# Performance work log

Hardware: AMD Instinct MI355X
Metric: run time of the kernel (lower is better)

## Reference

```python
import jax, jax.numpy as jnp
import numpy as np
from jax import lax

B, N, F_, K, C = 16, 64, 1024, 13, 2   # batch, channels, feat(time), conv kernel, classes
EPS_BN = 1e-5


def setup_inputs() -> dict:
    key = jax.random.key(0)
    ks = jax.random.split(key, 12)
    kf = 1.0 / np.sqrt(F_)   # torch uniform init bound for Linear(F,.) and w
    kn = 1.0 / np.sqrt(N)    # Conv1d(N,1,k=1) bound
    kk = 1.0 / np.sqrt(K)    # Conv1d(1,1,k=K) bound
    u = lambda k, shape, b: jax.random.uniform(k, shape, jnp.float32, -b, b)
    return {
        "x": jax.random.normal(ks[0], (B, N, F_), jnp.float32),
        "w": u(ks[1], (F_,), kf),
        "gin_W": u(ks[2], (F_, F_), kf),
        "gin_b": u(ks[3], (F_,), kf),
        "bn1_g": jnp.ones((N,), jnp.float32),
        "bn1_b": jnp.zeros((N,), jnp.float32),
        "lc_W": u(ks[4], (N,), kn),
        "lc_b": u(ks[5], (1,), kn),
        "conv_W": u(ks[6], (1, 1, K), kk),
        "conv_b": u(ks[7], (1,), kk),
        "bn2_g": jnp.ones((1,), jnp.float32),
        "bn2_b": jnp.zeros((1,), jnp.float32),
        "out_W": u(ks[8], (C, F_), kf),
        "out_b": u(ks[9], (C,), kf),
    }


def reference(x, w, gin_W, gin_b, bn1_g, bn1_b, lc_W, lc_b, conv_W, conv_b,
              bn2_g, bn2_b, out_W, out_b):
    # --- learned adjacency: weighted L1 pairwise score ---
    diff = jnp.abs(x[:, :, None, :] - x[:, None, :, :])        # [B,N,N,F] big intermediate
    s = jnp.einsum('bijf,f->bij', diff, w)                      # [B,N,N]
    s = -jax.nn.relu(s)
    adj = jax.nn.softmax(s, axis=1)                             # softmax over dim 1 (as torch)
    # --- GIN aggregation (eps=0): (adj + I) @ x, then Linear ---
    a = adj + jnp.eye(N, dtype=x.dtype)
    h = jnp.einsum('bij,bjf->bif', a, x)                        # [B,N,F]
    h = jnp.einsum('bif,of->bio', h, gin_W) + gin_b             # [B,N,F]
    # --- BatchNorm1d over channels (train-mode batch stats, biased var) ---
    m = h.mean(axis=(0, 2), keepdims=True)
    v = h.var(axis=(0, 2), keepdims=True)
    h = (h - m) / jnp.sqrt(v + EPS_BN) * bn1_g[None, :, None] + bn1_b[None, :, None]
    # --- Conv1d(N->1, k=1): channel mixing ---
    y = jnp.einsum('bnf,n->bf', h, lc_W) + lc_b                 # [B,F]
    # --- Conv1d(1->1, k=K, padding='same') ---
    y = lax.conv_general_dilated(y[:, None, :], conv_W, (1,), 'SAME') + conv_b[None, :, None]
    # --- BatchNorm1d(1) ---
    m2 = y.mean(axis=(0, 2), keepdims=True)
    v2 = y.var(axis=(0, 2), keepdims=True)
    y = (y - m2) / jnp.sqrt(v2 + EPS_BN) * bn2_g[None, :, None] + bn2_b[None, :, None]
    # --- head ---
    y = jax.nn.relu(y.reshape(B, F_))
    logits = y @ out_W.T + out_b                                # [B,C]
    return jax.nn.softmax(logits, axis=1), adj
```

## Files before the change

### kernel.cpp

```cpp
#include <hip/hip_runtime.h>
#include <hip/hip_bf16.h>


typedef __attribute__((ext_vector_type(8))) __bf16 bf16x8;
typedef __attribute__((ext_vector_type(4))) float f32x4;

__device__ __forceinline__ unsigned short f2bf(float f) {
  union { float f; unsigned int u; } v; v.f = f;
  unsigned int r = v.u + 0x7FFFu + ((v.u >> 16) & 1u);
  return (unsigned short)(r >> 16);
}

__global__ __launch_bounds__(256) void k1_spart_gemm(
    const float* __restrict__ x, const float* __restrict__ w,
    const float* __restrict__ gin_W,
    float* __restrict__ spart, float* __restrict__ gpart,
    unsigned* __restrict__ bar) {
  __shared__ __align__(16) union {
    struct { float xt[64 * 68]; float wt[64]; } s;
    struct { unsigned short A[64 * 72]; unsigned short B[64 * 72]; } g;
  } sm;
  int t = threadIdx.x, bid = blockIdx.x;

  if (bid == 0 && t == 0) *bar = 0u;

  if (bid >= 512) {
    int sbid = bid - 512;
    int b = sbid >> 4, ft = sbid & 15, f0 = ft * 64;
    const float4* pf = reinterpret_cast<const float4*>(gin_W) + (size_t)sbid * 1024 + t;
    float4 pf0 = pf[0], pf1 = pf[256], pf2 = pf[512], pf3 = pf[768];
    for (int c = 0; c < 16; ++c) {
      int idx = c * 256 + t;
      int n = idx >> 6, f = idx & 63;
      sm.s.xt[n * 68 + f] = x[b * 65536 + n * 1024 + f0 + f];
    }
    if (t < 64) sm.s.wt[t] = w[f0 + t];
    __syncthreads();
    asm volatile("" :: "v"(pf0.x), "v"(pf1.x), "v"(pf2.x), "v"(pf3.x));
    int i0 = (t >> 4) * 4, j0 = (t & 15) * 4;
    float acc[4][4];
#pragma unroll
    for (int ii = 0; ii < 4; ++ii)
#pragma unroll
      for (int jj = 0; jj < 4; ++jj) acc[ii][jj] = 0.f;
    for (int f = 0; f < 64; f += 4) {
      float4 wv = *reinterpret_cast<const float4*>(&sm.s.wt[f]);
      float4 av[4], bv[4];
#pragma unroll
      for (int ii = 0; ii < 4; ++ii) av[ii] = *reinterpret_cast<const float4*>(&sm.s.xt[(i0 + ii) * 68 + f]);
#pragma unroll
      for (int jj = 0; jj < 4; ++jj) bv[jj] = *reinterpret_cast<const float4*>(&sm.s.xt[(j0 + jj) * 68 + f]);
#pragma unroll
      for (int ii = 0; ii < 4; ++ii)
#pragma unroll
        for (int jj = 0; jj < 4; ++jj) {
          acc[ii][jj] += fabsf(av[ii].x - bv[jj].x) * wv.x
                       + fabsf(av[ii].y - bv[jj].y) * wv.y
                       + fabsf(av[ii].z - bv[jj].z) * wv.z
                       + fabsf(av[ii].w - bv[jj].w) * wv.w;
        }
    }
    float* out = spart + (size_t)sbid * 4096;
#pragma unroll
    for (int ii = 0; ii < 4; ++ii)
#pragma unroll
      for (int jj = 0; jj < 4; ++jj)
        out[(ii + i0) * 64 + (j0 + jj)] = acc[ii][jj];
    return;
  }

  int g = bid;
  int xcd = g & 7, idx = g >> 3;
  int lt = idx & 31, slice = idx >> 5;
  int tr = 4 * (xcd & 3) + (lt >> 3);
  int tc = 8 * (xcd >> 2) + (lt & 7);
  int k0 = slice * 512;
  int wave = t >> 6, lane = t & 63;
  int wr = wave * 16;
  int lrow = lane & 15, kg = lane >> 4;
  f32x4 acc[4];
#pragma unroll
  for (int nj = 0; nj < 4; ++nj) acc[nj] = f32x4{0.f, 0.f, 0.f, 0.f};

  for (int chunk = 0; chunk < 8; ++chunk) {
    int kc = k0 + chunk * 64;
#pragma unroll
    for (int u = 0; u < 4; ++u) {
      int idx4 = u * 256 + t;
      int row = idx4 >> 4, kq = idx4 & 15;
      float4 va = *reinterpret_cast<const float4*>(&x[(size_t)(tr * 64 + row) * 1024 + kc + kq * 4]);
      ushort4 ua; ua.x = f2bf(va.x); ua.y = f2bf(va.y); ua.z = f2bf(va.z); ua.w = f2bf(va.w);
      *reinterpret_cast<ushort4*>(&sm.g.A[row * 72 + kq * 4]) = ua;
    }
#pragma unroll
    for (int u = 0; u < 4; ++u) {
      int idx4 = u * 256 + t;
      int row = idx4 >> 4, kq = idx4 & 15;
      float4 vb = *reinterpret_cast<const float4*>(&gin_W[(size_t)(tc * 64 + row) * 1024 + kc + kq * 4]);
      ushort4 ub; ub.x = f2bf(vb.x); ub.y = f2bf(vb.y); ub.z = f2bf(vb.z); ub.w = f2bf(vb.w);
      *reinterpret_cast<ushort4*>(&sm.g.B[row * 72 + kq * 4]) = ub;
    }
    __syncthreads();
#pragma unroll
    for (int ks = 0; ks < 2; ++ks) {
      bf16x8 a = *reinterpret_cast<const bf16x8*>(&sm.g.A[(wr + lrow) * 72 + ks * 32 + kg * 8]);
      bf16x8 bf_[4];
#pragma unroll
      for (int nj = 0; nj < 4; ++nj)
        bf_[nj] = *reinterpret_cast<const bf16x8*>(&sm.g.B[(nj * 16 + lrow) * 72 + ks * 32 + kg * 8]);
#pragma unroll
      for (int nj = 0; nj < 4; ++nj)
        acc[nj] = __builtin_amdgcn_mfma_f32_16x16x32_bf16(a, bf_[nj], acc[nj], 0, 0, 0);
    }
    __syncthreads();
  }
  float* gp = gpart + (size_t)slice * (1024u * 1024u);
#pragma unroll
  for (int nj = 0; nj < 4; ++nj) {
    int row = tr * 64 + wr + kg * 4;
    int col = tc * 64 + nj * 16 + lrow;
#pragma unroll
    for (int r = 0; r < 4; ++r)
      gp[(size_t)(row + r) * 1024 + col] = acc[nj][r];
  }
}

__global__ __launch_bounds__(512) void k2_adj_h2(
    const float* __restrict__ spart, const float* __restrict__ gpart,
    const float* __restrict__ gin_b,
    float* __restrict__ dout, float* __restrict__ h2, float* __restrict__ part) {
  __shared__ float adjs[64 * 65];
  __shared__ float csum[32][64];
  __shared__ float cinv[64];
  __shared__ __align__(16) float gt[64 * 68];
  int t = threadIdx.x, bid = blockIdx.x;
  int xcd = bid & 7, local = bid >> 3;
  int b = (xcd << 1) | (local & 1);
  int ft = local >> 1;
  int f0 = ft * 64;
  {
    int i = t >> 4, fl = (t & 15) * 4;
#pragma unroll
    for (int c = 0; c < 2; ++c) {
      int row = c * 32 + i;
      const float* base = gpart + (size_t)(b * 64 + row) * 1024 + f0 + fl;
      float4 s0 = *reinterpret_cast<const float4*>(base);
      float4 s1 = *reinterpret_cast<const float4*>(base + (1u << 20));
      float4 g4;
      g4.x = s0.x + s1.x; g4.y = s0.y + s1.y;
      g4.z = s0.z + s1.z; g4.w = s0.w + s1.w;
      *reinterpret_cast<float4*>(&gt[row * 68 + fl]) = g4;
    }
  }
  int tj = t & 15, tr2 = t >> 4;
  float4 v4[2];
#pragma unroll
  for (int r = 0; r < 2; ++r) v4[r] = make_float4(0.f, 0.f, 0.f, 0.f);
  for (int ft2 = 0; ft2 < 16; ++ft2) {
    const float* p = spart + (size_t)(b * 16 + ft2) * 4096 + tj * 4;
#pragma unroll
    for (int r = 0; r < 2; ++r) {
      float4 s = *reinterpret_cast<const float4*>(&p[(tr2 * 2 + r) * 64]);
      v4[r].x += s.x; v4[r].y += s.y; v4[r].z += s.z; v4[r].w += s.w;
    }
  }
  float4 colsum = make_float4(0.f, 0.f, 0.f, 0.f);
#pragma unroll
  for (int r = 0; r < 2; ++r) {
    float4 e;
    e.x = expf(-fmaxf(v4[r].x, 0.f));
    e.y = expf(-fmaxf(v4[r].y, 0.f));
    e.z = expf(-fmaxf(v4[r].z, 0.f));
    e.w = expf(-fmaxf(v4[r].w, 0.f));
    int row = tr2 * 2 + r;
    adjs[row * 65 + tj * 4 + 0] = e.x;
    adjs[row * 65 + tj * 4 + 1] = e.y;
    adjs[row * 65 + tj * 4 + 2] = e.z;
    adjs[row * 65 + tj * 4 + 3] = e.w;
    colsum.x += e.x; colsum.y += e.y; colsum.z += e.z; colsum.w += e.w;
  }
  csum[tr2][tj * 4 + 0] = colsum.x;
  csum[tr2][tj * 4 + 1] = colsum.y;
  csum[tr2][tj * 4 + 2] = colsum.z;
  csum[tr2][tj * 4 + 3] = colsum.w;
  __syncthreads();
  if (t < 64) {
    float s = 0.f;
#pragma unroll
    for (int g2 = 0; g2 < 32; ++g2) s += csum[g2][t];
    cinv[t] = 1.f / s;
  }
  __syncthreads();
  float* doutAdj = dout + 32 + (size_t)b * 4096;
#pragma unroll
  for (int r = 0; r < 2; ++r) {
    int row = tr2 * 2 + r;
#pragma unroll
    for (int c = 0; c < 4; ++c) {
      int col = tj * 4 + c;
      float a = adjs[row * 65 + col] * cinv[col];
      adjs[row * 65 + col] = a;
      if (ft == 0) doutAdj[row * 64 + col] = a;
    }
  }
  __syncthreads();
  int i0 = (t >> 4) * 2, fl = (t & 15) * 4;
  float4 gbv = *reinterpret_cast<const float4*>(&gin_b[f0 + fl]);
  float4 acc4[2];
  acc4[0] = *reinterpret_cast<const float4*>(&gt[i0 * 68 + fl]);
  acc4[1] = *reinterpret_cast<const float4*>(&gt[(i0 + 1) * 68 + fl]);
  for (int j = 0; j < 64; ++j) {
    float4 gv = *reinterpret_cast<const float4*>(&gt[j * 68 + fl]);
    float a0 = adjs[i0 * 65 + j], a1 = adjs[(i0 + 1) * 65 + j];
    acc4[0].x += a0 * gv.x; acc4[0].y += a0 * gv.y; acc4[0].z += a0 * gv.z; acc4[0].w += a0 * gv.w;
    acc4[1].x += a1 * gv.x; acc4[1].y += a1 * gv.y; acc4[1].z += a1 * gv.z; acc4[1].w += a1 * gv.w;
  }
  float rs[2], rq[2];
#pragma unroll
  for (int ii = 0; ii < 2; ++ii) {
    acc4[ii].x += gbv.x; acc4[ii].y += gbv.y; acc4[ii].z += gbv.z; acc4[ii].w += gbv.w;
    *reinterpret_cast<float4*>(&h2[(size_t)(b * 64 + i0 + ii) * 1024 + f0 + fl]) = acc4[ii];
    rs[ii] = (acc4[ii].x + acc4[ii].y) + (acc4[ii].z + acc4[ii].w);
    rq[ii] = (acc4[ii].x * acc4[ii].x + acc4[ii].y * acc4[ii].y)
           + (acc4[ii].z * acc4[ii].z + acc4[ii].w * acc4[ii].w);
  }
#pragma unroll
  for (int m = 1; m < 16; m <<= 1) {
#pragma unroll
    for (int r = 0; r < 2; ++r) {
      rs[r] += __shfl_xor(rs[r], m, 64);
      rq[r] += __shfl_xor(rq[r], m, 64);
    }
  }
  if ((t & 15) == 0) {
    float* pp = part + (size_t)(b * 16 + ft) * 128;
#pragma unroll
    for (int r = 0; r < 2; ++r) {
      int n = i0 + r;
      pp[2 * n]     = rs[r];
      pp[2 * n + 1] = rq[r];
    }
  }
}

__global__ __launch_bounds__(256) void k3_y_head(
    const float* __restrict__ h2, const float* __restrict__ part,
    const float* __restrict__ lc_W, const float* __restrict__ lc_b,
    const float* __restrict__ bn1_g, const float* __restrict__ bn1_b,
    const float* __restrict__ conv_W, const float* __restrict__ conv_b,
    const float* __restrict__ bn2_g, const float* __restrict__ bn2_b,
    const float* __restrict__ out_W, const float* __restrict__ out_b,
    float* __restrict__ y2, float* __restrict__ bn2part,
    float* __restrict__ dout, unsigned* __restrict__ bar) {
  __shared__ float redp[2][128];
  __shared__ float cls[64], dds[64];
  __shared__ float yloc[268];
  __shared__ float red[256], red2[256];
  __shared__ float c0s;
  __shared__ unsigned tk;
  int t = threadIdx.x, bid = blockIdx.x;
  int b = ((bid & 7) << 1) | ((bid >> 3) & 1);
  int fq = bid >> 4;
  int f0 = fq * 256;
  {
    int k = t & 127, h = t >> 7;
    float s = 0.f;
    const float* pp = part + (size_t)h * 128 * 128 + k;
    for (int p = 0; p < 128; ++p) s += pp[(size_t)p * 128];
    redp[h][k] = s;
  }
  __syncthreads();
  if (t < 64) {
    float sum = redp[0][2 * t] + redp[1][2 * t];
    float sq  = redp[0][2 * t + 1] + redp[1][2 * t + 1];
    float m = sum * (1.f / 16384.f);
    float var = sq * (1.f / 16384.f) - m * m;
    float inv = 1.f / sqrtf(var + 1e-5f);
    float g = bn1_g[t], be = bn1_b[t], lw = lc_W[t];
    cls[t] = lw * g * inv;
    dds[t] = lw * (be - m * inv * g);
  }
  __syncthreads();
  if (t == 0) {
    float s = 0.f;
    for (int n = 0; n < 64; ++n) s += dds[n];
    c0s = s + lc_b[0];
  }
  __syncthreads();
  float c0 = c0s;
  for (int idx = t; idx < 268; idx += 256) {
    int f = f0 - 6 + idx;
    float acc = 0.f;
    if (f >= 0 && f < 1024) {
      acc = c0;
      const float* col = h2 + (size_t)(b * 64) * 1024 + f;
      for (int n = 0; n < 64; ++n) acc += cls[n] * col[(size_t)n * 1024];
    }
    yloc[idx] = acc;
  }
  __syncthreads();
  float cw[13];
#pragma unroll
  for (int k = 0; k < 13; ++k) cw[k] = conv_W[k];
  float vv = conv_b[0];
#pragma unroll
  for (int k = 0; k < 13; ++k) vv += yloc[t + k] * cw[k];
  y2[b * 1024 + f0 + t] = vv;
  red[t] = vv; red2[t] = vv * vv;
  __syncthreads();
  for (int off = 128; off > 0; off >>= 1) {
    if (t < off) { red[t] += red[t + off]; red2[t] += red2[t + off]; }
    __syncthreads();
  }
  if (t == 0) {
    int dchunk = b * 4 + fq;
    bn2part[2 * dchunk] = red[0]; bn2part[2 * dchunk + 1] = red2[0];
  }

  __syncthreads();
  if (t == 0) { __threadfence(); tk = atomicAdd(bar, 1u); }
  __syncthreads();
  if (tk != 63u) return;
  __threadfence();

  {
    float S = 0.f, S2 = 0.f;
    for (int i = 0; i < 64; ++i) { S += bn2part[2 * i]; S2 += bn2part[2 * i + 1]; }
    float m2 = S * (1.f / 16384.f);
    float inv2 = 1.f / sqrtf(S2 * (1.f / 16384.f) - m2 * m2 + 1e-5f);
    float g2 = bn2_g[0] * inv2, be2 = bn2_b[0];
    int hb = t >> 4, seg = t & 15;
    const float4* yv = reinterpret_cast<const float4*>(&y2[hb * 1024 + seg * 64]);
    const float4* w0 = reinterpret_cast<const float4*>(&out_W[seg * 64]);
    const float4* w1 = reinterpret_cast<const float4*>(&out_W[1024 + seg * 64]);
    float a0 = 0.f, a1 = 0.f;
#pragma unroll 4
    for (int u = 0; u < 16; ++u) {
      float4 y4 = yv[u], cc0 = w0[u], cc1 = w1[u];
      float vx = fmaxf((y4.x - m2) * g2 + be2, 0.f);
      float vy = fmaxf((y4.y - m2) * g2 + be2, 0.f);
      float vz = fmaxf((y4.z - m2) * g2 + be2, 0.f);
      float vw = fmaxf((y4.w - m2) * g2 + be2, 0.f);
      a0 += vx * cc0.x + vy * cc0.y + vz * cc0.z + vw * cc0.w;
      a1 += vx * cc1.x + vy * cc1.y + vz * cc1.z + vw * cc1.w;
    }
    red[t] = a0; red2[t] = a1;
    __syncthreads();
    for (int off = 8; off > 0; off >>= 1) {
      if (seg < off) { red[t] += red[t + off]; red2[t] += red2[t + off]; }
      __syncthreads();
    }
    if (seg == 0) {
      float l0 = red[t] + out_b[0], l1 = red2[t] + out_b[1];
      float mx = fmaxf(l0, l1);
      float e0 = expf(l0 - mx), e1 = expf(l1 - mx);
      float inv = 1.f / (e0 + e1);
      dout[hb * 2 + 0] = e0 * inv;
      dout[hb * 2 + 1] = e1 * inv;
    }
  }
}

extern "C" void kernel_launch(void* const* d_in, const int* in_sizes, int n_in,
                              void* d_out, int out_size, void* d_ws, size_t ws_size,
                              hipStream_t stream) {
  (void)in_sizes; (void)n_in; (void)out_size; (void)ws_size;
  const float* x      = (const float*)d_in[0];
  const float* w      = (const float*)d_in[1];
  const float* gin_W  = (const float*)d_in[2];
  const float* gin_b  = (const float*)d_in[3];
  const float* bn1_g  = (const float*)d_in[4];
  const float* bn1_b  = (const float*)d_in[5];
  const float* lc_W   = (const float*)d_in[6];
  const float* lc_b   = (const float*)d_in[7];
  const float* conv_W = (const float*)d_in[8];
  const float* conv_b = (const float*)d_in[9];
  const float* bn2_g  = (const float*)d_in[10];
  const float* bn2_b  = (const float*)d_in[11];
  const float* out_W  = (const float*)d_in[12];
  const float* out_b  = (const float*)d_in[13];
  float* dout = (float*)d_out;

  char* ws = (char*)d_ws;
  float* spart   = (float*)ws;
  float* h2      = (float*)(ws + (4u << 20));
  float* gpart   = (float*)(ws + (8u << 20));
  float* part    = (float*)(ws + (16u << 20));
  float* y2      = (float*)(ws + (16u << 20) + (128u << 10));
  float* bn2part = (float*)(ws + (16u << 20) + (192u << 10));
  unsigned* bar  = (unsigned*)(ws + (16u << 20) + (194u << 10));

  k1_spart_gemm<<<dim3(768), dim3(256), 0, stream>>>(x, w, gin_W, spart, gpart, bar);
  k2_adj_h2    <<<dim3(256), dim3(512), 0, stream>>>(spart, gpart, gin_b, dout, h2, part);
  k3_y_head    <<<dim3(64),  dim3(256), 0, stream>>>(h2, part, lc_W, lc_b, bn1_g, bn1_b,
                                                     conv_W, conv_b, bn2_g, bn2_b, out_W, out_b,
                                                     y2, bn2part, dout, bar);
}
```

Measured before the change: 64.01 us.

## Move BN1 stat reduction into k2 last-block and widen k3 grid

```diff
diff --git a/kernel.cpp b/kernel.cpp
--- a/kernel.cpp
+++ b/kernel.cpp
@@ -22,7 +22,7 @@
   } sm;
   int t = threadIdx.x, bid = blockIdx.x;
 
-  if (bid == 0 && t == 0) *bar = 0u;
+  if (bid == 0 && t == 0) { bar[0] = 0u; bar[16] = 0u; }
 
   if (bid >= 512) {
     int sbid = bid - 512;
@@ -65,7 +65,7 @@
     for (int ii = 0; ii < 4; ++ii)
 #pragma unroll
       for (int jj = 0; jj < 4; ++jj)
-        out[(ii + i0) * 64 + (j0 + jj)] = acc[ii][jj];
+        out[(i0 + ii) * 64 + (j0 + jj)] = acc[ii][jj];
     return;
   }
 
@@ -128,11 +128,14 @@
 __global__ __launch_bounds__(512) void k2_adj_h2(
     const float* __restrict__ spart, const float* __restrict__ gpart,
     const float* __restrict__ gin_b,
-    float* __restrict__ dout, float* __restrict__ h2, float* __restrict__ part) {
+    float* __restrict__ dout, float* __restrict__ h2, float* __restrict__ part,
+    float* __restrict__ stats, unsigned* __restrict__ bar) {
   __shared__ float adjs[64 * 65];
   __shared__ float csum[32][64];
   __shared__ float cinv[64];
   __shared__ __align__(16) float gt[64 * 68];
+  __shared__ float redps[4][128];
+  __shared__ unsigned tk;
   int t = threadIdx.x, bid = blockIdx.x;
   int xcd = bid & 7, local = bid >> 3;
   int b = (xcd << 1) | (local & 1);
@@ -241,10 +244,32 @@
       pp[2 * n + 1] = rq[r];
     }
   }
+
+  __syncthreads();
+  if (t == 0) { __threadfence(); tk = atomicAdd(&bar[16], 1u); }
+  __syncthreads();
+  if (tk != 255u) return;
+  __threadfence();
+  {
+    int slot = t & 127, quarter = t >> 7;
+    float s = 0.f;
+    const float* pp = part + (size_t)quarter * 64 * 128 + slot;
+    for (int p = 0; p < 64; ++p) s += pp[(size_t)p * 128];
+    redps[quarter][slot] = s;
+    __syncthreads();
+    if (t < 64) {
+      float sum = (redps[0][2 * t] + redps[1][2 * t]) + (redps[2][2 * t] + redps[3][2 * t]);
+      float sq  = (redps[0][2 * t + 1] + redps[1][2 * t + 1]) + (redps[2][2 * t + 1] + redps[3][2 * t + 1]);
+      float m = sum * (1.f / 16384.f);
+      float var = sq * (1.f / 16384.f) - m * m;
+      stats[2 * t]     = m;
+      stats[2 * t + 1] = 1.f / sqrtf(var + 1e-5f);
+    }
+  }
 }
 
 __global__ __launch_bounds__(256) void k3_y_head(
-    const float* __restrict__ h2, const float* __restrict__ part,
+    const float* __restrict__ h2, const float* __restrict__ stats,
     const float* __restrict__ lc_W, const float* __restrict__ lc_b,
     const float* __restrict__ bn1_g, const float* __restrict__ bn1_b,
     const float* __restrict__ conv_W, const float* __restrict__ conv_b,
@@ -252,30 +277,17 @@
     const float* __restrict__ out_W, const float* __restrict__ out_b,
     float* __restrict__ y2, float* __restrict__ bn2part,
     float* __restrict__ dout, unsigned* __restrict__ bar) {
-  __shared__ float redp[2][128];
   __shared__ float cls[64], dds[64];
-  __shared__ float yloc[268];
+  __shared__ float plds[4][76];
+  __shared__ float yloc[76];
   __shared__ float red[256], red2[256];
   __shared__ float c0s;
   __shared__ unsigned tk;
   int t = threadIdx.x, bid = blockIdx.x;
-  int b = ((bid & 7) << 1) | ((bid >> 3) & 1);
-  int fq = bid >> 4;
-  int f0 = fq * 256;
-  {
-    int k = t & 127, h = t >> 7;
-    float s = 0.f;
-    const float* pp = part + (size_t)h * 128 * 128 + k;
-    for (int p = 0; p < 128; ++p) s += pp[(size_t)p * 128];
-    redp[h][k] = s;
-  }
-  __syncthreads();
+  int b = bid >> 4, fq = bid & 15;
+  int f0 = fq * 64;
   if (t < 64) {
-    float sum = redp[0][2 * t] + redp[1][2 * t];
-    float sq  = redp[0][2 * t + 1] + redp[1][2 * t + 1];
-    float m = sum * (1.f / 16384.f);
-    float var = sq * (1.f / 16384.f) - m * m;
-    float inv = 1.f / sqrtf(var + 1e-5f);
+    float m = stats[2 * t], inv = stats[2 * t + 1];
     float g = bn1_g[t], be = bn1_b[t], lw = lc_W[t];
     cls[t] = lw * g * inv;
     dds[t] = lw * (be - m * inv * g);
@@ -287,48 +299,63 @@
     c0s = s + lc_b[0];
   }
   __syncthreads();
-  float c0 = c0s;
-  for (int idx = t; idx < 268; idx += 256) {
-    int f = f0 - 6 + idx;
-    float acc = 0.f;
-    if (f >= 0 && f < 1024) {
-      acc = c0;
-      const float* col = h2 + (size_t)(b * 64) * 1024 + f;
-      for (int n = 0; n < 64; ++n) acc += cls[n] * col[(size_t)n * 1024];
-    }
-    yloc[idx] = acc;
-  }
-  __syncthreads();
-  float cw[13];
-#pragma unroll
-  for (int k = 0; k < 13; ++k) cw[k] = conv_W[k];
-  float vv = conv_b[0];
-#pragma unroll
-  for (int k = 0; k < 13; ++k) vv += yloc[t + k] * cw[k];
-  y2[b * 1024 + f0 + t] = vv;
-  red[t] = vv; red2[t] = vv * vv;
-  __syncthreads();
-  for (int off = 128; off > 0; off >>= 1) {
-    if (t < off) { red[t] += red[t + off]; red2[t] += red2[t + off]; }
-    __syncthreads();
-  }
-  if (t == 0) {
-    int dchunk = b * 4 + fq;
-    bn2part[2 * dchunk] = red[0]; bn2part[2 * dchunk + 1] = red2[0];
-  }
-
-  __syncthreads();
-  if (t == 0) { __threadfence(); tk = atomicAdd(bar, 1u); }
-  __syncthreads();
-  if (tk != 63u) return;
+  {
+    int q = t >> 6, il = t & 63;
+    for (int idx = il; idx < 76; idx += 64) {
+      int f = f0 - 6 + idx;
+      float acc = 0.f;
+      if (f >= 0 && f < 1024) {
+        const float* col = h2 + (size_t)(b * 64) * 1024 + f;
+#pragma unroll
+        for (int n = 0; n < 16; ++n) acc += cls[q * 16 + n] * col[(size_t)(q * 16 + n) * 1024];
+      }
+      plds[q][idx] = acc;
+    }
+  }
+  __syncthreads();
+  if (t < 76) {
+    int f = f0 - 6 + t;
+    float v = 0.f;
+    if (f >= 0 && f < 1024)
+      v = c0s + ((plds[0][t] + plds[1][t]) + (plds[2][t] + plds[3][t]));
+    yloc[t] = v;
+  }
+  __syncthreads();
+  if (t < 64) {
+    float cw[13];
+#pragma unroll
+    for (int k = 0; k < 13; ++k) cw[k] = conv_W[k];
+    float vv = conv_b[0];
+#pragma unroll
+    for (int k = 0; k < 13; ++k) vv += yloc[t + k] * cw[k];
+    y2[b * 1024 + f0 + t] = vv;
+    float s = vv, s2 = vv * vv;
+#pragma unroll
+    for (int m = 1; m < 64; m <<= 1) {
+      s  += __shfl_xor(s, m, 64);
+      s2 += __shfl_xor(s2, m, 64);
+    }
+    if (t == 0) { bn2part[2 * bid] = s; bn2part[2 * bid + 1] = s2; }
+  }
+
+  __syncthreads();
+  if (t == 0) { __threadfence(); tk = atomicAdd(&bar[0], 1u); }
+  __syncthreads();
+  if (tk != 255u) return;
   __threadfence();
 
   {
-    float S = 0.f, S2 = 0.f;
-    for (int i = 0; i < 64; ++i) { S += bn2part[2 * i]; S2 += bn2part[2 * i + 1]; }
+    red[t] = bn2part[2 * t]; red2[t] = bn2part[2 * t + 1];
+    __syncthreads();
+    for (int off = 128; off > 0; off >>= 1) {
+      if (t < off) { red[t] += red[t + off]; red2[t] += red2[t + off]; }
+      __syncthreads();
+    }
+    float S = red[0], S2 = red2[0];
     float m2 = S * (1.f / 16384.f);
     float inv2 = 1.f / sqrtf(S2 * (1.f / 16384.f) - m2 * m2 + 1e-5f);
     float g2 = bn2_g[0] * inv2, be2 = bn2_b[0];
+    __syncthreads();
     int hb = t >> 4, seg = t & 15;
     const float4* yv = reinterpret_cast<const float4*>(&y2[hb * 1024 + seg * 64]);
     const float4* w0 = reinterpret_cast<const float4*>(&out_W[seg * 64]);
@@ -388,11 +415,13 @@
   float* part    = (float*)(ws + (16u << 20));
   float* y2      = (float*)(ws + (16u << 20) + (128u << 10));
   float* bn2part = (float*)(ws + (16u << 20) + (192u << 10));
-  unsigned* bar  = (unsigned*)(ws + (16u << 20) + (194u << 10));
+  float* stats   = (float*)(ws + (16u << 20) + (194u << 10));
+  unsigned* bar  = (unsigned*)(ws + (16u << 20) + (195u << 10));
 
   k1_spart_gemm<<<dim3(768), dim3(256), 0, stream>>>(x, w, gin_W, spart, gpart, bar);
-  k2_adj_h2    <<<dim3(256), dim3(512), 0, stream>>>(spart, gpart, gin_b, dout, h2, part);
-  k3_y_head    <<<dim3(64),  dim3(256), 0, stream>>>(h2, part, lc_W, lc_b, bn1_g, bn1_b,
+  k2_adj_h2    <<<dim3(256), dim3(512), 0, stream>>>(spart, gpart, gin_b, dout, h2, part,
+                                                     stats, bar);
+  k3_y_head    <<<dim3(256), dim3(256), 0, stream>>>(h2, stats, lc_W, lc_b, bn1_g, bn1_b,
                                                      conv_W, conv_b, bn2_g, bn2_b, out_W, out_b,
                                                      y2, bn2part, dout, bar);
 }
```

Result: faster. 57.61 us (-10.0%).
